# Kernel optimization log

Measured on AMD Instinct MI355X. Metric: run time of the kernel, lower is better.

## Reference

```python
import jax, jax.numpy as jnp
import numpy as np

H = 128  # hidden_size
I = 28   # input_size
C = 10   # num_classes


def setup_inputs() -> dict:
    key = jax.random.key(0)
    ks = jax.random.split(key, 11)
    s = 1.0 / np.sqrt(H)  # torch nn.RNN init scale
    return {
        "x": jax.random.normal(ks[0], (8192, 28, I), dtype=jnp.float32),
        "W_ih0": jax.random.uniform(ks[1], (H, I), jnp.float32, -s, s),
        "W_hh0": jax.random.uniform(ks[2], (H, H), jnp.float32, -s, s),
        "b_ih0": jax.random.uniform(ks[3], (H,), jnp.float32, -s, s),
        "b_hh0": jax.random.uniform(ks[4], (H,), jnp.float32, -s, s),
        "W_ih1": jax.random.uniform(ks[5], (H, H), jnp.float32, -s, s),
        "W_hh1": jax.random.uniform(ks[6], (H, H), jnp.float32, -s, s),
        "b_ih1": jax.random.uniform(ks[7], (H,), jnp.float32, -s, s),
        "b_hh1": jax.random.uniform(ks[8], (H,), jnp.float32, -s, s),
        "fc_w": jax.random.uniform(ks[9], (C, H), jnp.float32, -s, s),
        "fc_b": jax.random.uniform(ks[10], (C,), jnp.float32, -s, s),
    }


def _rnn_layer_full(x, W_ih, b_ih, W_hh, b_hh):
    # x: [B, T, D] -> full output sequence [B, T, H]
    B = x.shape[0]
    h0 = jnp.zeros((B, H), x.dtype)
    xw = jnp.einsum('btd,hd->bth', x, W_ih) + b_ih  # precompute input GEMM

    def step(h, xw_t):
        h = jnp.tanh(xw_t + h @ W_hh.T + b_hh)
        return h, h

    _, ys = jax.lax.scan(step, h0, jnp.swapaxes(xw, 0, 1))  # [T, B, H]
    return jnp.swapaxes(ys, 0, 1)


def _rnn_layer_last(x, W_ih, b_ih, W_hh, b_hh):
    # only the final hidden state is needed downstream
    B = x.shape[0]
    h0 = jnp.zeros((B, H), x.dtype)
    xw = jnp.einsum('btd,hd->bth', x, W_ih) + b_ih

    def step(h, xw_t):
        h = jnp.tanh(xw_t + h @ W_hh.T + b_hh)
        return h, None

    h_last, _ = jax.lax.scan(step, h0, jnp.swapaxes(xw, 0, 1))
    return h_last


def reference(x, W_ih0, W_hh0, b_ih0, b_hh0, W_ih1, W_hh1, b_ih1, b_hh1, fc_w, fc_b):
    out0 = _rnn_layer_full(x, W_ih0, b_ih0, W_hh0, b_hh0)   # [B, T, H]
    h_last = _rnn_layer_last(out0, W_ih1, b_ih1, W_hh1, b_hh1)  # [B, H] == out[:, -1, :]
    return h_last @ fc_w.T + fc_b  # [B, C]
```

## Files before the change

### kernel.cpp

```cpp
#include <hip/hip_runtime.h>

#define HSZ 128
#define ISZ 28
#define TSZ 28
#define CSZ 10
#define BT  16
#define NT  512
#define HP  136
#define XP  32

typedef _Float16 half_t;
typedef _Float16 v8h __attribute__((ext_vector_type(8)));
typedef _Float16 v4h __attribute__((ext_vector_type(4)));
typedef float v4f __attribute__((ext_vector_type(4)));

__device__ __forceinline__ float fast_tanh(float x) {
    float e = __expf(2.f * x);
    return 1.f - 2.f * __builtin_amdgcn_rcpf(e + 1.f);
}

__global__ __launch_bounds__(NT, 4)
void rnn_mfma3(const float* __restrict__ x,
               const float* __restrict__ W_ih0, const float* __restrict__ W_hh0,
               const float* __restrict__ b_ih0, const float* __restrict__ b_hh0,
               const float* __restrict__ W_ih1, const float* __restrict__ W_hh1,
               const float* __restrict__ b_ih1, const float* __restrict__ b_hh1,
               const float* __restrict__ fc_w, const float* __restrict__ fc_b,
               float* __restrict__ out)
{
    __shared__ half_t h0s[2][BT * HP];
    __shared__ half_t h1s[2][BT * HP];
    __shared__ half_t xss[2][BT * XP];

    const int tid  = threadIdx.x;
    const int wave = tid >> 6;
    const int lane = tid & 63;
    const int ln   = lane & 15;
    const int quad = lane >> 4;
    const int kq   = quad * 8;
    const int b0   = blockIdx.x * BT;
    const int base = wave * 16;
    const int row  = base + ln;

    v8h aWx, aW0[4], aW1i[4], aW1h[4];
    v4f bias0, bias1;
    {
        float4 p = *(const float4*)(b_ih0 + base + quad * 4);
        float4 q = *(const float4*)(b_hh0 + base + quad * 4);
        bias0 = (v4f){p.x + q.x, p.y + q.y, p.z + q.z, p.w + q.w};
        p = *(const float4*)(b_ih1 + base + quad * 4);
        q = *(const float4*)(b_hh1 + base + quad * 4);
        bias1 = (v4f){p.x + q.x, p.y + q.y, p.z + q.z, p.w + q.w};
    }
    {
        const float* pw = W_ih0 + row * ISZ + kq;
        float4 a = *(const float4*)pw;
        float4 b = (kq < 24) ? *(const float4*)(pw + 4) : make_float4(0.f, 0.f, 0.f, 0.f);
        aWx = (v8h){(half_t)a.x, (half_t)a.y, (half_t)a.z, (half_t)a.w,
                    (half_t)b.x, (half_t)b.y, (half_t)b.z, (half_t)b.w};
    }
#pragma unroll
    for (int ks = 0; ks < 4; ++ks) {
        const float4* p0 = (const float4*)(W_hh0 + row * HSZ + ks * 32 + kq);
        const float4* p1 = (const float4*)(W_ih1 + row * HSZ + ks * 32 + kq);
        const float4* p2 = (const float4*)(W_hh1 + row * HSZ + ks * 32 + kq);
        float4 a = p0[0], b = p0[1];
        aW0[ks] = (v8h){(half_t)a.x, (half_t)a.y, (half_t)a.z, (half_t)a.w,
                        (half_t)b.x, (half_t)b.y, (half_t)b.z, (half_t)b.w};
        a = p1[0]; b = p1[1];
        aW1i[ks] = (v8h){(half_t)a.x, (half_t)a.y, (half_t)a.z, (half_t)a.w,
                         (half_t)b.x, (half_t)b.y, (half_t)b.z, (half_t)b.w};
        a = p2[0]; b = p2[1];
        aW1h[ks] = (v8h){(half_t)a.x, (half_t)a.y, (half_t)a.z, (half_t)a.w,
                         (half_t)b.x, (half_t)b.y, (half_t)b.z, (half_t)b.w};
    }

    const int  xm  = tid >> 5;
    const int  xi  = tid & 31;
    const bool xok = xi < ISZ;
    const float* xrow = x + (size_t)(b0 + xm) * (TSZ * ISZ) + xi;

    xss[0][xm * XP + xi] = (half_t)(xok ? xrow[0] : 0.f);
    xss[1][xm * XP + xi] = (half_t)(xok ? xrow[ISZ] : 0.f);
    float xcur = xok ? xrow[2 * ISZ] : 0.f;

    for (int idx = tid; idx < BT * HP; idx += NT)
        h1s[0][idx] = (half_t)0.f;
    __syncthreads();

    {
        const v8h bx = *(const v8h*)&xss[0][ln * XP + kq];
        v4f a0 = bias0;
        a0 = __builtin_amdgcn_mfma_f32_16x16x32_f16(aWx, bx, a0, 0, 0, 0);
        v4h p = {(half_t)fast_tanh(a0[0]), (half_t)fast_tanh(a0[1]),
                 (half_t)fast_tanh(a0[2]), (half_t)fast_tanh(a0[3])};
        *(v4h*)&h0s[0][ln * HP + base + quad * 4] = p;
    }
    __syncthreads();

    for (int t = 0; t < TSZ - 1; ++t) {
        const int pr = t & 1;

        float xnew = 0.f;
        if (t < TSZ - 3 && xok) xnew = xrow[(t + 3) * ISZ];

        v8h bh0[4];
#pragma unroll
        for (int ks = 0; ks < 4; ++ks)
            bh0[ks] = *(const v8h*)&h0s[pr][ln * HP + ks * 32 + kq];
        const v8h bx = *(const v8h*)&xss[pr ^ 1][ln * XP + kq];

        v4f a1 = bias1, a0 = bias0;
        a0 = __builtin_amdgcn_mfma_f32_16x16x32_f16(aWx, bx, a0, 0, 0, 0);
#pragma unroll
        for (int ks = 0; ks < 4; ++ks) {
            const v8h bh1 = *(const v8h*)&h1s[pr][ln * HP + ks * 32 + kq];
            a1 = __builtin_amdgcn_mfma_f32_16x16x32_f16(aW1i[ks], bh0[ks], a1, 0, 0, 0);
            a1 = __builtin_amdgcn_mfma_f32_16x16x32_f16(aW1h[ks], bh1,     a1, 0, 0, 0);
            a0 = __builtin_amdgcn_mfma_f32_16x16x32_f16(aW0[ks],  bh0[ks], a0, 0, 0, 0);
        }

        {
            v4h p1 = {(half_t)fast_tanh(a1[0]), (half_t)fast_tanh(a1[1]),
                      (half_t)fast_tanh(a1[2]), (half_t)fast_tanh(a1[3])};
            *(v4h*)&h1s[pr ^ 1][ln * HP + base + quad * 4] = p1;
            v4h p0 = {(half_t)fast_tanh(a0[0]), (half_t)fast_tanh(a0[1]),
                      (half_t)fast_tanh(a0[2]), (half_t)fast_tanh(a0[3])};
            *(v4h*)&h0s[pr ^ 1][ln * HP + base + quad * 4] = p0;
        }

        if (t < TSZ - 2)
            xss[pr][xm * XP + xi] = (half_t)xcur;
        xcur = xnew;

        __syncthreads();
    }

    {
        const int pr = (TSZ - 1) & 1;
        v4f a1 = bias1;
#pragma unroll
        for (int ks = 0; ks < 4; ++ks) {
            const v8h bh0 = *(const v8h*)&h0s[pr][ln * HP + ks * 32 + kq];
            const v8h bh1 = *(const v8h*)&h1s[pr][ln * HP + ks * 32 + kq];
            a1 = __builtin_amdgcn_mfma_f32_16x16x32_f16(aW1i[ks], bh0, a1, 0, 0, 0);
            a1 = __builtin_amdgcn_mfma_f32_16x16x32_f16(aW1h[ks], bh1, a1, 0, 0, 0);
        }
        v4h p1 = {(half_t)fast_tanh(a1[0]), (half_t)fast_tanh(a1[1]),
                  (half_t)fast_tanh(a1[2]), (half_t)fast_tanh(a1[3])};
        *(v4h*)&h1s[pr ^ 1][ln * HP + base + quad * 4] = p1;
    }
    __syncthreads();

    if (tid < BT * CSZ) {
        const int m = tid / CSZ, cc = tid - m * CSZ;
        float s = fc_b[cc];
#pragma unroll
        for (int k8 = 0; k8 < HSZ / 8; ++k8) {
            const v8h hv = *(const v8h*)&h1s[0][m * HP + k8 * 8];
            const float4 w0 = *(const float4*)(fc_w + cc * HSZ + k8 * 8);
            const float4 w1 = *(const float4*)(fc_w + cc * HSZ + k8 * 8 + 4);
            s += (float)hv[0] * w0.x + (float)hv[1] * w0.y +
                 (float)hv[2] * w0.z + (float)hv[3] * w0.w +
                 (float)hv[4] * w1.x + (float)hv[5] * w1.y +
                 (float)hv[6] * w1.z + (float)hv[7] * w1.w;
        }
        out[(b0 + m) * CSZ + cc] = s;
    }
}

extern "C" void kernel_launch(void* const* d_in, const int* in_sizes, int n_in,
                              void* d_out, int out_size, void* d_ws, size_t ws_size,
                              hipStream_t stream) {
    const float* x     = (const float*)d_in[0];
    const float* W_ih0 = (const float*)d_in[1];
    const float* W_hh0 = (const float*)d_in[2];
    const float* b_ih0 = (const float*)d_in[3];
    const float* b_hh0 = (const float*)d_in[4];
    const float* W_ih1 = (const float*)d_in[5];
    const float* W_hh1 = (const float*)d_in[6];
    const float* b_ih1 = (const float*)d_in[7];
    const float* b_hh1 = (const float*)d_in[8];
    const float* fc_w  = (const float*)d_in[9];
    const float* fc_b  = (const float*)d_in[10];
    float* out = (float*)d_out;

    const int B = in_sizes[0] / (TSZ * ISZ);
    dim3 grid(B / BT), block(NT);
    rnn_mfma3<<<grid, block, 0, stream>>>(x, W_ih0, W_hh0, b_ih0, b_hh0,
                                          W_ih1, W_hh1, b_ih1, b_hh1,
                                          fc_w, fc_b, out);
}
```

Baseline: 130.0 us.

## Preload whole x tile to LDS upfront and split layer-1 MFMA accumulator chains

New measurement: 126.9 us (median of 3 runs). -2.4%, faster.

```diff
diff --git a/kernel.cpp b/kernel.cpp
--- a/kernel.cpp
+++ b/kernel.cpp
@@ -20,7 +20,7 @@
 }
 
 __global__ __launch_bounds__(NT, 4)
-void rnn_mfma3(const float* __restrict__ x,
+void rnn_mfma4(const float* __restrict__ x,
                const float* __restrict__ W_ih0, const float* __restrict__ W_hh0,
                const float* __restrict__ b_ih0, const float* __restrict__ b_hh0,
                const float* __restrict__ W_ih1, const float* __restrict__ W_hh1,
@@ -30,7 +30,7 @@
 {
     __shared__ half_t h0s[2][BT * HP];
     __shared__ half_t h1s[2][BT * HP];
-    __shared__ half_t xss[2][BT * XP];
+    __shared__ half_t xs[TSZ][BT * XP];
 
     const int tid  = threadIdx.x;
     const int wave = tid >> 6;
@@ -75,21 +75,34 @@
                          (half_t)b.x, (half_t)b.y, (half_t)b.z, (half_t)b.w};
     }
 
-    const int  xm  = tid >> 5;
-    const int  xi  = tid & 31;
-    const bool xok = xi < ISZ;
-    const float* xrow = x + (size_t)(b0 + xm) * (TSZ * ISZ) + xi;
-
-    xss[0][xm * XP + xi] = (half_t)(xok ? xrow[0] : 0.f);
-    xss[1][xm * XP + xi] = (half_t)(xok ? xrow[ISZ] : 0.f);
-    float xcur = xok ? xrow[2 * ISZ] : 0.f;
+    {
+        const float* xblk = x + (size_t)b0 * (TSZ * ISZ);
+#pragma unroll
+        for (int k = 0; k < 7; ++k) {
+            const int F = tid + k * NT;
+            if (F < BT * 196) {
+                const int r   = F / 196;
+                const int rem = F - r * 196;
+                const int t   = rem / 7;
+                const int i4  = (rem - t * 7) * 4;
+                const float4 v = *(const float4*)(xblk + r * (TSZ * ISZ) + rem * 4);
+                v4h p = {(half_t)v.x, (half_t)v.y, (half_t)v.z, (half_t)v.w};
+                *(v4h*)&xs[t][r * XP + i4] = p;
+            }
+        }
+        if (tid < TSZ * BT) {
+            const int tt = tid >> 4, rr = tid & 15;
+            *(v4h*)&xs[tt][rr * XP + ISZ] =
+                (v4h){(half_t)0.f, (half_t)0.f, (half_t)0.f, (half_t)0.f};
+        }
+    }
 
     for (int idx = tid; idx < BT * HP; idx += NT)
         h1s[0][idx] = (half_t)0.f;
     __syncthreads();
 
     {
-        const v8h bx = *(const v8h*)&xss[0][ln * XP + kq];
+        const v8h bx = *(const v8h*)&xs[0][ln * XP + kq];
         v4f a0 = bias0;
         a0 = __builtin_amdgcn_mfma_f32_16x16x32_f16(aWx, bx, a0, 0, 0, 0);
         v4h p = {(half_t)fast_tanh(a0[0]), (half_t)fast_tanh(a0[1]),
@@ -98,27 +111,29 @@
     }
     __syncthreads();
 
+#pragma unroll 2
     for (int t = 0; t < TSZ - 1; ++t) {
         const int pr = t & 1;
 
-        float xnew = 0.f;
-        if (t < TSZ - 3 && xok) xnew = xrow[(t + 3) * ISZ];
-
-        v8h bh0[4];
-#pragma unroll
-        for (int ks = 0; ks < 4; ++ks)
+        v8h bh0[4], bh1[4];
+#pragma unroll
+        for (int ks = 0; ks < 4; ++ks) {
             bh0[ks] = *(const v8h*)&h0s[pr][ln * HP + ks * 32 + kq];
-        const v8h bx = *(const v8h*)&xss[pr ^ 1][ln * XP + kq];
-
-        v4f a1 = bias1, a0 = bias0;
+            bh1[ks] = *(const v8h*)&h1s[pr][ln * HP + ks * 32 + kq];
+        }
+        const v8h bx = *(const v8h*)&xs[t + 1][ln * XP + kq];
+
+        v4f a0  = bias0;
+        v4f a1i = bias1;
+        v4f a1h = (v4f){0.f, 0.f, 0.f, 0.f};
         a0 = __builtin_amdgcn_mfma_f32_16x16x32_f16(aWx, bx, a0, 0, 0, 0);
 #pragma unroll
         for (int ks = 0; ks < 4; ++ks) {
-            const v8h bh1 = *(const v8h*)&h1s[pr][ln * HP + ks * 32 + kq];
-            a1 = __builtin_amdgcn_mfma_f32_16x16x32_f16(aW1i[ks], bh0[ks], a1, 0, 0, 0);
-            a1 = __builtin_amdgcn_mfma_f32_16x16x32_f16(aW1h[ks], bh1,     a1, 0, 0, 0);
-            a0 = __builtin_amdgcn_mfma_f32_16x16x32_f16(aW0[ks],  bh0[ks], a0, 0, 0, 0);
-        }
+            a1i = __builtin_amdgcn_mfma_f32_16x16x32_f16(aW1i[ks], bh0[ks], a1i, 0, 0, 0);
+            a1h = __builtin_amdgcn_mfma_f32_16x16x32_f16(aW1h[ks], bh1[ks], a1h, 0, 0, 0);
+            a0  = __builtin_amdgcn_mfma_f32_16x16x32_f16(aW0[ks],  bh0[ks], a0,  0, 0, 0);
+        }
+        const v4f a1 = a1i + a1h;
 
         {
             v4h p1 = {(half_t)fast_tanh(a1[0]), (half_t)fast_tanh(a1[1]),
@@ -129,23 +144,21 @@
             *(v4h*)&h0s[pr ^ 1][ln * HP + base + quad * 4] = p0;
         }
 
-        if (t < TSZ - 2)
-            xss[pr][xm * XP + xi] = (half_t)xcur;
-        xcur = xnew;
-
         __syncthreads();
     }
 
     {
         const int pr = (TSZ - 1) & 1;
-        v4f a1 = bias1;
+        v4f a1i = bias1;
+        v4f a1h = (v4f){0.f, 0.f, 0.f, 0.f};
 #pragma unroll
         for (int ks = 0; ks < 4; ++ks) {
             const v8h bh0 = *(const v8h*)&h0s[pr][ln * HP + ks * 32 + kq];
             const v8h bh1 = *(const v8h*)&h1s[pr][ln * HP + ks * 32 + kq];
-            a1 = __builtin_amdgcn_mfma_f32_16x16x32_f16(aW1i[ks], bh0, a1, 0, 0, 0);
-            a1 = __builtin_amdgcn_mfma_f32_16x16x32_f16(aW1h[ks], bh1, a1, 0, 0, 0);
-        }
+            a1i = __builtin_amdgcn_mfma_f32_16x16x32_f16(aW1i[ks], bh0, a1i, 0, 0, 0);
+            a1h = __builtin_amdgcn_mfma_f32_16x16x32_f16(aW1h[ks], bh1, a1h, 0, 0, 0);
+        }
+        const v4f a1 = a1i + a1h;
         v4h p1 = {(half_t)fast_tanh(a1[0]), (half_t)fast_tanh(a1[1]),
                   (half_t)fast_tanh(a1[2]), (half_t)fast_tanh(a1[3])};
         *(v4h*)&h1s[pr ^ 1][ln * HP + base + quad * 4] = p1;
@@ -187,7 +200,7 @@
 
     const int B = in_sizes[0] / (TSZ * ISZ);
     dim3 grid(B / BT), block(NT);
-    rnn_mfma3<<<grid, block, 0, stream>>>(x, W_ih0, W_hh0, b_ih0, b_hh0,
+    rnn_mfma4<<<grid, block, 0, stream>>>(x, W_ih0, W_hh0, b_ih0, b_hh0,
                                           W_ih1, W_hh1, b_ih1, b_hh1,
                                           fc_w, fc_b, out);
 }
```
